# Kernel tuning notes

Measured on AMD Instinct MI355X. Metric: run time of the kernel, lower is better.

## Reference

```python
import jax, jax.numpy as jnp
import numpy as np


def _chord_mask(n):
    # Chord-protocol sparsity: mask[i, i] = 1 and mask[i, (i + 2**j) % n] = 1
    m = np.zeros((n, n), dtype=np.float32)
    idx = np.arange(n)
    m[idx, idx] = 1.0
    for j in range(int(np.log2(n))):
        m[idx, (idx + 2 ** j) % n] = 1.0
    return jnp.asarray(m)


def setup_inputs() -> dict:
    key = jax.random.key(0)
    ks = jax.random.split(key, 8)
    B, n_vec, n_dim = 16, 1024, 64
    n_hidden, n_W, n_class = 32, 10, 10
    data = jax.random.normal(ks[0], (B, n_vec, n_dim), dtype=jnp.float32)
    s1 = 1.0 / np.sqrt(n_dim)
    s2 = 1.0 / np.sqrt(n_hidden)
    s3 = 1.0 / np.sqrt(n_vec * n_dim)
    fW1 = jax.random.uniform(ks[1], (n_W, n_dim, n_hidden), jnp.float32, -s1, s1)
    fb1 = jax.random.uniform(ks[2], (n_W, n_hidden), jnp.float32, -s1, s1)
    fW2 = jax.random.uniform(ks[3], (n_W, n_hidden, n_vec), jnp.float32, -s2, s2)
    fb2 = jax.random.uniform(ks[4], (n_W, n_vec), jnp.float32, -s2, s2)
    final_W = jax.random.uniform(ks[5], (n_vec * n_dim, n_class), jnp.float32, -s3, s3)
    final_b = jax.random.uniform(ks[6], (n_class,), jnp.float32, -s3, s3)
    return {"data": data, "fW1": fW1, "fb1": fb1, "fW2": fW2, "fb2": fb2,
            "final_W": final_W, "final_b": final_b}


def reference(data, fW1, fb1, fW2, fb2, final_W, final_b):
    B, n_vec, n_dim = data.shape
    n_W = fW1.shape[0]
    mask = _chord_mask(n_vec)  # [n_vec, n_vec], static constant
    V = data
    residual = V
    # fs[::-1] -> iterate layers in reverse order
    for i in range(n_W - 1, -1, -1):
        h = jax.nn.gelu(jnp.einsum('bnd,dh->bnh', data, fW1[i]) + fb1[i],
                        approximate=False)
        W = jnp.einsum('bnh,hm->bnm', h, fW2[i]) + fb2[i]  # [B, n_vec, n_vec]
        W = W * mask
        V = jnp.einsum('bnm,bmd->bnd', W, V) + residual
        residual = V  # residual_every=True
    flat = V.reshape(B, n_vec * n_dim)
    return flat @ final_W + final_b
```

## Files before the change

kernel.cpp:

```cpp
#include <hip/hip_runtime.h>

#define BATCH 16
#define NVEC 1024
#define NDIM 64
#define NHID 32
#define NW   10
#define NCLS 10
#define NOFF 11
#define WPAD 12

__global__ __launch_bounds__(256) void k_transpose(
    const float* __restrict__ fW2, float* __restrict__ W2T)
{
    __shared__ float tile[NHID][65];
    const int i = blockIdx.y;
    const int m0 = blockIdx.x * 64;
    const int t = threadIdx.x;
    const int tL = t & 63, wv = t >> 6;

    const float* src = fW2 + (size_t)i * NHID * NVEC;
    #pragma unroll
    for (int jj = 0; jj < 8; ++jj) {
        int j = wv * 8 + jj;
        tile[j][tL] = src[(size_t)j * NVEC + m0 + tL];
    }
    __syncthreads();

    float* dst = W2T + (size_t)i * NVEC * NHID;
    const int j = t & 31, mrow = t >> 5;
    #pragma unroll
    for (int g = 0; g < 8; ++g) {
        int m = g * 8 + mrow;
        dst[(size_t)(m0 + m) * NHID + j] = tile[j][m];
    }
}

__global__ __launch_bounds__(256, 1) void k_weights(
    const float* __restrict__ data,
    const float* __restrict__ fW1,
    const float* __restrict__ fb1,
    const float* __restrict__ W2T,
    const float* __restrict__ fb2,
    float* __restrict__ Wsp)
{
    const int i  = blockIdx.y;
    const int t  = threadIdx.x;
    const int nl = t & 15;
    const int b  = t >> 4;
    const int n  = blockIdx.x * 16 + nl;

    const float* w1 = fW1 + (size_t)i * NDIM * NHID;
    const float* b1 = fb1 + (size_t)i * NHID;
    float h[NHID];
    #pragma unroll
    for (int j = 0; j < NHID; ++j) h[j] = b1[j];

    const float4* arow = (const float4*)(data + ((size_t)(b * NVEC) + n) * NDIM);
    #pragma unroll 2
    for (int g = 0; g < 16; ++g) {
        float4 a = arow[g];
        float xs[4] = {a.x, a.y, a.z, a.w};
        #pragma unroll
        for (int dk = 0; dk < 4; ++dk) {
            float x = xs[dk];
            const float* wr = w1 + (g * 4 + dk) * NHID;
            #pragma unroll
            for (int j = 0; j < NHID; ++j) h[j] += x * wr[j];
        }
    }

    #pragma unroll
    for (int j = 0; j < NHID; ++j) {
        float x = h[j];
        h[j] = 0.5f * x * (1.0f + erff(x * 0.70710678118654752f));
    }

    const float* w2t = W2T + (size_t)i * NVEC * NHID;
    const float* b2  = fb2 + (size_t)i * NVEC;
    float* wout = Wsp + ((size_t)(i * BATCH + b) * NVEC + n) * WPAD;
    #pragma unroll 1
    for (int o = 0; o < NOFF; ++o) {
        int off = (o == 0) ? 0 : (1 << (o - 1));
        int m = (n + off) & (NVEC - 1);
        const float4* gp = (const float4*)(w2t + (size_t)m * NHID);
        float acc = b2[m];
        #pragma unroll
        for (int k = 0; k < 8; ++k) {
            float4 gv = gp[k];
            acc += h[k * 4 + 0] * gv.x + h[k * 4 + 1] * gv.y
                 + h[k * 4 + 2] * gv.z + h[k * 4 + 3] * gv.w;
        }
        wout[o] = acc;
    }
}

__global__ __launch_bounds__(1024) void k_chain(
    const float* __restrict__ data,
    const float* __restrict__ Wsp,
    const float* __restrict__ Wf,
    float* __restrict__ part)
{
    const int chunk = blockIdx.x;
    const int b     = blockIdx.y;
    const int d0    = chunk * 4;
    const int n     = threadIdx.x;

    __shared__ float4 bufA[NVEC];
    __shared__ float4 bufB[NVEC];

    bufA[n] = *(const float4*)(data + ((size_t)(b * NVEC) + n) * NDIM + d0);

    const float4* wp = (const float4*)(Wsp + ((size_t)((NW - 1) * BATCH + b) * NVEC + n) * WPAD);
    float4 wa = wp[0], wb4 = wp[1], wc = wp[2];
    __syncthreads();

    float4* cur = bufA;
    float4* nxt = bufB;

    for (int l = 0; l < NW; ++l) {
        float4 na, nb, nc;
        if (l < NW - 1) {
            const float4* wpn = (const float4*)(
                Wsp + ((size_t)((NW - 2 - l) * BATCH + b) * NVEC + n) * WPAD);
            na = wpn[0]; nb = wpn[1]; nc = wpn[2];
        }
        const float wgt[12] = {wa.x, wa.y, wa.z, wa.w,
                               wb4.x, wb4.y, wb4.z, wb4.w,
                               wc.x, wc.y, wc.z, wc.w};
        float4 v0 = cur[n];
        float4 acc;
        acc.x = v0.x + wgt[0] * v0.x;
        acc.y = v0.y + wgt[0] * v0.y;
        acc.z = v0.z + wgt[0] * v0.z;
        acc.w = v0.w + wgt[0] * v0.w;
        #pragma unroll
        for (int o = 1; o < NOFF; ++o) {
            int off = 1 << (o - 1);
            float4 vv = cur[(n + off) & (NVEC - 1)];
            acc.x += wgt[o] * vv.x; acc.y += wgt[o] * vv.y;
            acc.z += wgt[o] * vv.z; acc.w += wgt[o] * vv.w;
        }
        nxt[n] = acc;
        __syncthreads();
        float4* tmp = cur; cur = nxt; nxt = tmp;
        if (l < NW - 1) { wa = na; wb4 = nb; wc = nc; }
    }

    float p[NCLS];
    #pragma unroll
    for (int c = 0; c < NCLS; ++c) p[c] = 0.0f;
    {
        float4 vv = cur[n];
        float vs[4] = {vv.x, vv.y, vv.z, vv.w};
        const float4* wfv = (const float4*)(Wf + ((size_t)(n * NDIM + d0)) * NCLS);
        float wf[40];
        #pragma unroll
        for (int k = 0; k < 10; ++k) {
            float4 u = wfv[k];
            wf[k * 4 + 0] = u.x; wf[k * 4 + 1] = u.y;
            wf[k * 4 + 2] = u.z; wf[k * 4 + 3] = u.w;
        }
        #pragma unroll
        for (int d = 0; d < 4; ++d)
            #pragma unroll
            for (int cls = 0; cls < NCLS; ++cls)
                p[cls] += vs[d] * wf[d * NCLS + cls];
    }

    const int lane = n & 63, wv = n >> 6;
    float* sred = (float*)nxt;
    #pragma unroll
    for (int cls = 0; cls < NCLS; ++cls) {
        float v = p[cls];
        #pragma unroll
        for (int s = 32; s > 0; s >>= 1) v += __shfl_down(v, s, 64);
        if (lane == 0) sred[wv * NCLS + cls] = v;
    }
    __syncthreads();
    if (n < NCLS) {
        float s = 0.0f;
        #pragma unroll
        for (int w = 0; w < 16; ++w) s += sred[w * NCLS + n];
        part[(size_t)(b * 16 + chunk) * NCLS + n] = s;
    }
}

__global__ __launch_bounds__(256) void k_finish(
    const float* __restrict__ part, const float* __restrict__ bias,
    float* __restrict__ out)
{
    int t = threadIdx.x;
    if (t < BATCH * NCLS) {
        int b = t / NCLS, cls = t % NCLS;
        float s = bias[cls];
        #pragma unroll
        for (int ch = 0; ch < 16; ++ch) s += part[(size_t)(b * 16 + ch) * NCLS + cls];
        out[t] = s;
    }
}

extern "C" void kernel_launch(void* const* d_in, const int* in_sizes, int n_in,
                              void* d_out, int out_size, void* d_ws, size_t ws_size,
                              hipStream_t stream) {
    const float* data = (const float*)d_in[0];
    const float* fW1  = (const float*)d_in[1];
    const float* fb1  = (const float*)d_in[2];
    const float* fW2  = (const float*)d_in[3];
    const float* fb2  = (const float*)d_in[4];
    const float* fWf  = (const float*)d_in[5];
    const float* fbf  = (const float*)d_in[6];
    float* out = (float*)d_out;

    float* ws   = (float*)d_ws;
    float* Wsp  = ws;
    float* W2T  = Wsp + (size_t)NW * BATCH * NVEC * WPAD;
    float* part = W2T + (size_t)NW * NVEC * NHID;

    k_transpose<<<dim3(NVEC / 64, NW), 256, 0, stream>>>(fW2, W2T);
    k_weights<<<dim3(NVEC / 16, NW), 256, 0, stream>>>(
        data, fW1, fb1, W2T, fb2, Wsp);
    k_chain<<<dim3(NDIM / 4, BATCH), 1024, 0, stream>>>(data, Wsp, fWf, part);
    k_finish<<<dim3(1), 256, 0, stream>>>(part, fbf, out);
}
```

Measured before the change: 143.0 us.

## Split hidden dimension across waves in k_weights and reduce via shared memory

Each thread of k_weights now computes 8 of the 32 hidden units rather than all of them, with the four waves of a block covering the four hidden slices. Partial dot products for the 11 chord offsets are combined through a shared-memory array before being written out. The grid grows from 64 to 256 blocks in x, and the launch bound moves from 1 to 4 blocks per CU. The goal is to cut per-thread register pressure and serial work, and to raise occupancy and block count. The cost is each data row being read by four waves, plus an extra barrier and a shared-memory reduction.

```diff
diff --git a/kernel.cpp b/kernel.cpp
--- a/kernel.cpp
+++ b/kernel.cpp
@@ -35,7 +35,7 @@
     }
 }
 
-__global__ __launch_bounds__(256, 1) void k_weights(
+__global__ __launch_bounds__(256, 4) void k_weights(
     const float* __restrict__ data,
     const float* __restrict__ fW1,
     const float* __restrict__ fb1,
@@ -43,54 +43,68 @@
     const float* __restrict__ fb2,
     float* __restrict__ Wsp)
 {
-    const int i  = blockIdx.y;
-    const int t  = threadIdx.x;
-    const int nl = t & 15;
-    const int b  = t >> 4;
-    const int n  = blockIdx.x * 16 + nl;
-
-    const float* w1 = fW1 + (size_t)i * NDIM * NHID;
-    const float* b1 = fb1 + (size_t)i * NHID;
-    float h[NHID];
-    #pragma unroll
-    for (int j = 0; j < NHID; ++j) h[j] = b1[j];
+    const int i    = blockIdx.y;
+    const int t    = threadIdx.x;
+    const int lane = t & 63;
+    const int jq   = __builtin_amdgcn_readfirstlane(t >> 6);
+    const int j0   = jq * 8;
+    const int nb   = blockIdx.x & 63;
+    const int bb   = blockIdx.x >> 6;
+    const int nl   = lane & 15;
+    const int bq   = lane >> 4;
+    const int n    = nb * 16 + nl;
+    const int b    = bb * 4 + bq;
+
+    __shared__ float comb[NOFF * 4][64];
+
+    const float* w1 = fW1 + (size_t)i * NDIM * NHID + j0;
+    const float* b1 = fb1 + (size_t)i * NHID + j0;
+    float h[8];
+    #pragma unroll
+    for (int jj = 0; jj < 8; ++jj) h[jj] = b1[jj];
 
     const float4* arow = (const float4*)(data + ((size_t)(b * NVEC) + n) * NDIM);
-    #pragma unroll 2
+    #pragma unroll 4
     for (int g = 0; g < 16; ++g) {
         float4 a = arow[g];
         float xs[4] = {a.x, a.y, a.z, a.w};
         #pragma unroll
         for (int dk = 0; dk < 4; ++dk) {
+            const float* wr = w1 + (g * 4 + dk) * NHID;
             float x = xs[dk];
-            const float* wr = w1 + (g * 4 + dk) * NHID;
             #pragma unroll
-            for (int j = 0; j < NHID; ++j) h[j] += x * wr[j];
-        }
-    }
-
-    #pragma unroll
-    for (int j = 0; j < NHID; ++j) {
-        float x = h[j];
-        h[j] = 0.5f * x * (1.0f + erff(x * 0.70710678118654752f));
-    }
-
-    const float* w2t = W2T + (size_t)i * NVEC * NHID;
+            for (int jj = 0; jj < 8; ++jj) h[jj] += x * wr[jj];
+        }
+    }
+
+    #pragma unroll
+    for (int jj = 0; jj < 8; ++jj) {
+        float x = h[jj];
+        h[jj] = 0.5f * x * (1.0f + erff(x * 0.70710678118654752f));
+    }
+
+    const float* w2t = W2T + (size_t)i * NVEC * NHID + j0;
     const float* b2  = fb2 + (size_t)i * NVEC;
-    float* wout = Wsp + ((size_t)(i * BATCH + b) * NVEC + n) * WPAD;
-    #pragma unroll 1
+    #pragma unroll
     for (int o = 0; o < NOFF; ++o) {
-        int off = (o == 0) ? 0 : (1 << (o - 1));
+        int off = (1 << o) >> 1;
         int m = (n + off) & (NVEC - 1);
         const float4* gp = (const float4*)(w2t + (size_t)m * NHID);
-        float acc = b2[m];
-        #pragma unroll
-        for (int k = 0; k < 8; ++k) {
-            float4 gv = gp[k];
-            acc += h[k * 4 + 0] * gv.x + h[k * 4 + 1] * gv.y
-                 + h[k * 4 + 2] * gv.z + h[k * 4 + 3] * gv.w;
-        }
-        wout[o] = acc;
+        float4 g0 = gp[0], g1 = gp[1];
+        float p = h[0] * g0.x + h[1] * g0.y + h[2] * g0.z + h[3] * g0.w
+                + h[4] * g1.x + h[5] * g1.y + h[6] * g1.z + h[7] * g1.w;
+        if ((o & 3) == jq) p += b2[m];
+        comb[o * 4 + jq][lane] = p;
+    }
+    __syncthreads();
+
+    for (int idx = t; idx < NOFF * 64; idx += 256) {
+        int o = idx >> 6, row = idx & 63;
+        float s = comb[o * 4 + 0][row] + comb[o * 4 + 1][row]
+                + comb[o * 4 + 2][row] + comb[o * 4 + 3][row];
+        int rn = nb * 16 + (row & 15);
+        int rb = bb * 4 + (row >> 4);
+        Wsp[((size_t)(i * BATCH + rb) * NVEC + rn) * WPAD + o] = s;
     }
 }
 
@@ -217,7 +231,7 @@
     float* part = W2T + (size_t)NW * NVEC * NHID;
 
     k_transpose<<<dim3(NVEC / 64, NW), 256, 0, stream>>>(fW2, W2T);
-    k_weights<<<dim3(NVEC / 16, NW), 256, 0, stream>>>(
+    k_weights<<<dim3(256, NW), 256, 0, stream>>>(
         data, fW1, fb1, W2T, fb2, Wsp);
     k_chain<<<dim3(NDIM / 4, BATCH), 1024, 0, stream>>>(data, Wsp, fWf, part);
     k_finish<<<dim3(1), 256, 0, stream>>>(part, fbf, out);
```

Measured after the change: 146.1 us. 1.02x slower.

## Split hidden-layer GELU computation into separate kernel and use SoA chord weight layout

Applied to the files above, without the earlier changes.

The fused weights kernel, which held 32 hidden values per thread at low occupancy, is split in two. A new k_hidden kernel computes the GELU hidden activations with an LDS-transposed data tile, 8 outputs per thread and more parallelism. A second kernel reads them back from a new global H buffer and produces the 11 chord weights. The chord weight buffer also moves from a padded per-row AoS layout to an offset-major SoA layout, giving coalesced writes and reads. In exchange, the hidden buffer (about 21 MB) makes an extra round trip through global memory.

```diff
diff --git a/kernel.cpp b/kernel.cpp
--- a/kernel.cpp
+++ b/kernel.cpp
@@ -7,7 +7,7 @@
 #define NW   10
 #define NCLS 10
 #define NOFF 11
-#define WPAD 12
+#define NROWS (BATCH * NVEC)
 
 __global__ __launch_bounds__(256) void k_transpose(
     const float* __restrict__ fW2, float* __restrict__ W2T)
@@ -35,10 +35,66 @@
     }
 }
 
-__global__ __launch_bounds__(256, 1) void k_weights(
+__global__ __launch_bounds__(256) void k_hidden(
     const float* __restrict__ data,
     const float* __restrict__ fW1,
     const float* __restrict__ fb1,
+    float* __restrict__ H)
+{
+    const int i = blockIdx.y;
+    const int flat0 = blockIdx.x * 64;
+    const int t = threadIdx.x;
+
+    __shared__ float dT[NDIM][65];
+
+    {
+        const float4* src = (const float4*)(data + (size_t)flat0 * NDIM);
+        #pragma unroll
+        for (int q = 0; q < 4; ++q) {
+            int fidx = t + 256 * q;
+            int r  = fidx >> 4;
+            int d4 = fidx & 15;
+            float4 u = src[fidx];
+            dT[d4 * 4 + 0][r] = u.x;
+            dT[d4 * 4 + 1][r] = u.y;
+            dT[d4 * 4 + 2][r] = u.z;
+            dT[d4 * 4 + 3][r] = u.w;
+        }
+    }
+    __syncthreads();
+
+    const int r  = t & 63;
+    const int jq = t >> 6;
+    const int j0 = jq * 8;
+
+    const float* w1 = fW1 + (size_t)i * NDIM * NHID + j0;
+    const float* b1 = fb1 + (size_t)i * NHID + j0;
+
+    float h[8];
+    #pragma unroll
+    for (int jj = 0; jj < 8; ++jj) h[jj] = b1[jj];
+
+    #pragma unroll 8
+    for (int d = 0; d < NDIM; ++d) {
+        float x = dT[d][r];
+        const float* wr = w1 + d * NHID;
+        #pragma unroll
+        for (int jj = 0; jj < 8; ++jj) h[jj] += x * wr[jj];
+    }
+
+    #pragma unroll
+    for (int jj = 0; jj < 8; ++jj) {
+        float x = h[jj];
+        h[jj] = 0.5f * x * (1.0f + erff(x * 0.70710678118654752f));
+    }
+
+    float4* hp = (float4*)(H + ((size_t)i * NROWS + flat0 + r) * NHID + j0);
+    hp[0] = make_float4(h[0], h[1], h[2], h[3]);
+    hp[1] = make_float4(h[4], h[5], h[6], h[7]);
+}
+
+__global__ __launch_bounds__(256) void k_gatherw(
+    const float* __restrict__ H,
     const float* __restrict__ W2T,
     const float* __restrict__ fb2,
     float* __restrict__ Wsp)
@@ -49,48 +105,32 @@
     const int b  = t >> 4;
     const int n  = blockIdx.x * 16 + nl;
 
-    const float* w1 = fW1 + (size_t)i * NDIM * NHID;
-    const float* b1 = fb1 + (size_t)i * NHID;
-    float h[NHID];
-    #pragma unroll
-    for (int j = 0; j < NHID; ++j) h[j] = b1[j];
-
-    const float4* arow = (const float4*)(data + ((size_t)(b * NVEC) + n) * NDIM);
-    #pragma unroll 2
-    for (int g = 0; g < 16; ++g) {
-        float4 a = arow[g];
-        float xs[4] = {a.x, a.y, a.z, a.w};
-        #pragma unroll
-        for (int dk = 0; dk < 4; ++dk) {
-            float x = xs[dk];
-            const float* wr = w1 + (g * 4 + dk) * NHID;
-            #pragma unroll
-            for (int j = 0; j < NHID; ++j) h[j] += x * wr[j];
-        }
-    }
-
-    #pragma unroll
-    for (int j = 0; j < NHID; ++j) {
-        float x = h[j];
-        h[j] = 0.5f * x * (1.0f + erff(x * 0.70710678118654752f));
+    const float4* hp = (const float4*)(H + ((size_t)i * NROWS + b * NVEC + n) * NHID);
+    float hh[NHID];
+    #pragma unroll
+    for (int k = 0; k < 8; ++k) {
+        float4 u = hp[k];
+        hh[k * 4 + 0] = u.x; hh[k * 4 + 1] = u.y;
+        hh[k * 4 + 2] = u.z; hh[k * 4 + 3] = u.w;
     }
 
     const float* w2t = W2T + (size_t)i * NVEC * NHID;
     const float* b2  = fb2 + (size_t)i * NVEC;
-    float* wout = Wsp + ((size_t)(i * BATCH + b) * NVEC + n) * WPAD;
-    #pragma unroll 1
+    float* wout = Wsp + ((size_t)(i * BATCH + b) * NOFF) * NVEC + n;
+
+    #pragma unroll
     for (int o = 0; o < NOFF; ++o) {
-        int off = (o == 0) ? 0 : (1 << (o - 1));
+        int off = (1 << o) >> 1;
         int m = (n + off) & (NVEC - 1);
         const float4* gp = (const float4*)(w2t + (size_t)m * NHID);
         float acc = b2[m];
         #pragma unroll
         for (int k = 0; k < 8; ++k) {
-            float4 gv = gp[k];
-            acc += h[k * 4 + 0] * gv.x + h[k * 4 + 1] * gv.y
-                 + h[k * 4 + 2] * gv.z + h[k * 4 + 3] * gv.w;
-        }
-        wout[o] = acc;
+            float4 g = gp[k];
+            acc += hh[k * 4 + 0] * g.x + hh[k * 4 + 1] * g.y
+                 + hh[k * 4 + 2] * g.z + hh[k * 4 + 3] * g.w;
+        }
+        wout[o * NVEC] = acc;
     }
 }
 
@@ -110,40 +150,44 @@
 
     bufA[n] = *(const float4*)(data + ((size_t)(b * NVEC) + n) * NDIM + d0);
 
-    const float4* wp = (const float4*)(Wsp + ((size_t)((NW - 1) * BATCH + b) * NVEC + n) * WPAD);
-    float4 wa = wp[0], wb4 = wp[1], wc = wp[2];
+    float w[NOFF];
+    {
+        const float* wb = Wsp + ((size_t)((NW - 1) * BATCH + b) * NOFF) * NVEC + n;
+        #pragma unroll
+        for (int o = 0; o < NOFF; ++o) w[o] = wb[o * NVEC];
+    }
     __syncthreads();
 
     float4* cur = bufA;
     float4* nxt = bufB;
 
     for (int l = 0; l < NW; ++l) {
-        float4 na, nb, nc;
+        float nw[NOFF];
         if (l < NW - 1) {
-            const float4* wpn = (const float4*)(
-                Wsp + ((size_t)((NW - 2 - l) * BATCH + b) * NVEC + n) * WPAD);
-            na = wpn[0]; nb = wpn[1]; nc = wpn[2];
-        }
-        const float wgt[12] = {wa.x, wa.y, wa.z, wa.w,
-                               wb4.x, wb4.y, wb4.z, wb4.w,
-                               wc.x, wc.y, wc.z, wc.w};
+            const float* wb = Wsp + ((size_t)((NW - 2 - l) * BATCH + b) * NOFF) * NVEC + n;
+            #pragma unroll
+            for (int o = 0; o < NOFF; ++o) nw[o] = wb[o * NVEC];
+        }
         float4 v0 = cur[n];
         float4 acc;
-        acc.x = v0.x + wgt[0] * v0.x;
-        acc.y = v0.y + wgt[0] * v0.y;
-        acc.z = v0.z + wgt[0] * v0.z;
-        acc.w = v0.w + wgt[0] * v0.w;
+        acc.x = v0.x + w[0] * v0.x;
+        acc.y = v0.y + w[0] * v0.y;
+        acc.z = v0.z + w[0] * v0.z;
+        acc.w = v0.w + w[0] * v0.w;
         #pragma unroll
         for (int o = 1; o < NOFF; ++o) {
             int off = 1 << (o - 1);
             float4 vv = cur[(n + off) & (NVEC - 1)];
-            acc.x += wgt[o] * vv.x; acc.y += wgt[o] * vv.y;
-            acc.z += wgt[o] * vv.z; acc.w += wgt[o] * vv.w;
+            acc.x += w[o] * vv.x; acc.y += w[o] * vv.y;
+            acc.z += w[o] * vv.z; acc.w += w[o] * vv.w;
         }
         nxt[n] = acc;
         __syncthreads();
         float4* tmp = cur; cur = nxt; nxt = tmp;
-        if (l < NW - 1) { wa = na; wb4 = nb; wc = nc; }
+        if (l < NW - 1) {
+            #pragma unroll
+            for (int o = 0; o < NOFF; ++o) w[o] = nw[o];
+        }
     }
 
     float p[NCLS];
@@ -180,7 +224,7 @@
     if (n < NCLS) {
         float s = 0.0f;
         #pragma unroll
-        for (int w = 0; w < 16; ++w) s += sred[w * NCLS + n];
+        for (int w2 = 0; w2 < 16; ++w2) s += sred[w2 * NCLS + n];
         part[(size_t)(b * 16 + chunk) * NCLS + n] = s;
     }
 }
@@ -213,12 +257,13 @@
 
     float* ws   = (float*)d_ws;
     float* Wsp  = ws;
-    float* W2T  = Wsp + (size_t)NW * BATCH * NVEC * WPAD;
-    float* part = W2T + (size_t)NW * NVEC * NHID;
+    float* W2T  = Wsp + (size_t)NW * BATCH * NOFF * NVEC;
+    float* H    = W2T + (size_t)NW * NVEC * NHID;
+    float* part = H + (size_t)NW * NROWS * NHID;
 
     k_transpose<<<dim3(NVEC / 64, NW), 256, 0, stream>>>(fW2, W2T);
-    k_weights<<<dim3(NVEC / 16, NW), 256, 0, stream>>>(
-        data, fW1, fb1, W2T, fb2, Wsp);
+    k_hidden<<<dim3(NROWS / 64, NW), 256, 0, stream>>>(data, fW1, fb1, H);
+    k_gatherw<<<dim3(NVEC / 16, NW), 256, 0, stream>>>(H, W2T, fb2, Wsp);
     k_chain<<<dim3(NDIM / 4, BATCH), 1024, 0, stream>>>(data, Wsp, fWf, part);
     k_finish<<<dim3(1), 256, 0, stream>>>(part, fbf, out);
 }
```

Result: slower. 172.6 us (+20.7%).
